# Performance work log

Hardware: AMD Instinct MI355X
Metric: run time of the kernel (lower is better)

## Reference

```python
import jax, jax.numpy as jnp
import numpy as np


def setup_inputs() -> dict:
    key = jax.random.key(0)
    ks = jax.random.split(key, 4)
    B, T, D, U = 64, 2048, 128, 128
    enc = jax.random.normal(ks[0], (B, T, D), dtype=jnp.float32)
    # Keras Dense default: glorot_uniform kernel, zero bias; use scaled normals here.
    W1_w = jax.random.normal(ks[1], (D, U), dtype=jnp.float32) / np.sqrt(D)
    W2_w = jax.random.normal(ks[2], (D, U), dtype=jnp.float32) / np.sqrt(D)
    V_w = jax.random.normal(ks[3], (U, 1), dtype=jnp.float32) / np.sqrt(U)
    return {
        "encoder_outputs": enc,
        "W1_w": W1_w,
        "W1_b": jnp.zeros((U,), jnp.float32),
        "W2_w": W2_w,
        "W2_b": jnp.zeros((U,), jnp.float32),
        "V_w": V_w,
        "V_b": jnp.zeros((1,), jnp.float32),
    }


def reference(encoder_outputs, W1_w, W1_b, W2_w, W2_b, V_w, V_b):
    # score = V(tanh(W1(x) + W2(x)))  -> [B, T, 1]
    # W1(x)+W2(x) == x @ (W1_w + W2_w) + (W1_b + W2_b); keep faithful but fused.
    h = jnp.tanh(jnp.einsum("btd,du->btu", encoder_outputs, W1_w) + W1_b
                 + jnp.einsum("btd,du->btu", encoder_outputs, W2_w) + W2_b)
    score = jnp.einsum("btu,uo->bto", h, V_w) + V_b  # [B, T, 1]
    attn = jax.nn.softmax(score, axis=1)             # softmax over sequence axis
    # context = sum_t attn[b,t,0] * x[b,t,:]
    context = jnp.einsum("bto,btd->bd", attn, encoder_outputs)
    return context
```

## Files before the change

kernel.cpp:

```cpp
#include <hip/hip_runtime.h>
#include <hip/hip_bf16.h>

#define DD 128
#define UU 128
#define SEQ_T 2048
#define ROWS 64
#define PART_STRIDE 132

typedef __attribute__((ext_vector_type(8))) short short8;
typedef __attribute__((ext_vector_type(4))) float f32x4;

__device__ __forceinline__ unsigned short f2bf(float f) {
  unsigned u = __float_as_uint(f);
  u += 0x7fffu + ((u >> 16) & 1u);
  return (unsigned short)(u >> 16);
}
__device__ __forceinline__ float bf2f(unsigned short s) {
  return __uint_as_float(((unsigned)s) << 16);
}
__device__ __forceinline__ float fast_tanh(float v) {
  float z = __expf(2.0f * v);
  return 1.0f - __fdividef(2.0f, z + 1.0f);
}

__global__ void prep_kernel(const float* __restrict__ W1w, const float* __restrict__ W1b,
                            const float* __restrict__ W2w, const float* __restrict__ W2b,
                            unsigned short* __restrict__ wt_g, float* __restrict__ bias_g)
{
  int i = blockIdx.x * 256 + threadIdx.x;
  int u = i >> 7, d = i & 127;
  float s = W1w[(size_t)d * UU + u] + W2w[(size_t)d * UU + u];
  wt_g[(size_t)u * DD + d] = f2bf(s);
  if (i < UU) bias_g[i] = W1b[i] + W2b[i];
}

__global__ __launch_bounds__(256, 4)
void fused_score_ctx(const float* __restrict__ x,
                     const unsigned short* __restrict__ wt_g,
                     const float* __restrict__ bias_g,
                     const float* __restrict__ Vw,
                     float* __restrict__ part)
{
  __shared__ __align__(16) unsigned short xs[ROWS * DD];
  __shared__ __align__(16) float spart[4][ROWS];
  __shared__ float slds[ROWS];
  __shared__ __align__(16) float pctx_red[4][DD];

  const int tid = threadIdx.x;
  const int blk = blockIdx.x;
  const int rowbase = blk * ROWS;
  const int w = tid >> 6, l = tid & 63, lx = l & 15, lq = l >> 4;

  float4 xr[8];
  #pragma unroll
  for (int it = 0; it < 4; ++it) {
    int F = tid + 256 * it;
    int row = F >> 4, g = F & 15;
    const float* src = x + (size_t)(rowbase + row) * DD + g * 8;
    xr[2 * it]     = *reinterpret_cast<const float4*>(src);
    xr[2 * it + 1] = *reinterpret_cast<const float4*>(src + 4);
  }

  short8 Bf[2][4];
  float vs[2], bs[2];
  #pragma unroll
  for (int nf = 0; nf < 2; ++nf) {
    const int u = 32 * w + 16 * nf + lx;
    vs[nf] = Vw[u];
    bs[nf] = bias_g[u];
    #pragma unroll
    for (int kf = 0; kf < 4; ++kf)
      Bf[nf][kf] = *reinterpret_cast<const short8*>(
          wt_g + (size_t)u * DD + 32 * kf + 8 * lq);
  }

  #pragma unroll
  for (int it = 0; it < 4; ++it) {
    int F = tid + 256 * it;
    int row = F >> 4, g = F & 15;
    float4 v0 = xr[2 * it], v1 = xr[2 * it + 1];
    short8 pk;
    pk[0] = (short)f2bf(v0.x); pk[1] = (short)f2bf(v0.y);
    pk[2] = (short)f2bf(v0.z); pk[3] = (short)f2bf(v0.w);
    pk[4] = (short)f2bf(v1.x); pk[5] = (short)f2bf(v1.y);
    pk[6] = (short)f2bf(v1.z); pk[7] = (short)f2bf(v1.w);
    *reinterpret_cast<short8*>(xs + row * DD + ((g ^ (row & 15)) << 3)) = pk;
  }
  __syncthreads();

  f32x4 acc[4][2];
  #pragma unroll
  for (int mf = 0; mf < 4; ++mf) {
    acc[mf][0] = (f32x4){0.f, 0.f, 0.f, 0.f};
    acc[mf][1] = (f32x4){0.f, 0.f, 0.f, 0.f};
  }
  #pragma unroll
  for (int kf = 0; kf < 4; ++kf) {
    const int gs8 = ((4 * kf + lq) ^ lx) << 3;
    #pragma unroll
    for (int mf = 0; mf < 4; ++mf) {
      short8 a = *reinterpret_cast<const short8*>(xs + (16 * mf + lx) * DD + gs8);
      acc[mf][0] = __builtin_amdgcn_mfma_f32_16x16x32_bf16(a, Bf[0][kf], acc[mf][0], 0, 0, 0);
      acc[mf][1] = __builtin_amdgcn_mfma_f32_16x16x32_bf16(a, Bf[1][kf], acc[mf][1], 0, 0, 0);
    }
  }

  #pragma unroll
  for (int mf = 0; mf < 4; ++mf) {
    #pragma unroll
    for (int r = 0; r < 4; ++r) {
      float p = vs[0] * fast_tanh(acc[mf][0][r] + bs[0])
              + vs[1] * fast_tanh(acc[mf][1][r] + bs[1]);
      p += __shfl_xor(p, 1);
      p += __shfl_xor(p, 2);
      p += __shfl_xor(p, 4);
      p += __shfl_xor(p, 8);
      if (lx == 0) spart[w][16 * mf + 4 * lq + r] = p;
    }
  }
  __syncthreads();

  float sv = (spart[0][l] + spart[1][l]) + (spart[2][l] + spart[3][l]);
  float m = sv;
  #pragma unroll
  for (int off = 1; off < 64; off <<= 1) m = fmaxf(m, __shfl_xor(m, off));
  float e = __expf(sv - m);
  float lsum = e;
  #pragma unroll
  for (int off = 1; off < 64; off <<= 1) lsum += __shfl_xor(lsum, off);
  if (w == 0) slds[l] = e;
  __syncthreads();

  {
    const int gd = tid & 15;
    const int tg = tid >> 4;
    float ca[8];
    #pragma unroll
    for (int e2 = 0; e2 < 8; ++e2) ca[e2] = 0.0f;
    #pragma unroll
    for (int k = 0; k < 4; ++k) {
      int t = tg * 4 + k;
      float wgt = slds[t];
      short8 xv = *reinterpret_cast<const short8*>(xs + t * DD + ((gd ^ (t & 15)) << 3));
      #pragma unroll
      for (int e2 = 0; e2 < 8; ++e2)
        ca[e2] = fmaf(wgt, bf2f((unsigned short)xv[e2]), ca[e2]);
    }
    #pragma unroll
    for (int e2 = 0; e2 < 8; ++e2) {
      ca[e2] += __shfl_xor(ca[e2], 16);
      ca[e2] += __shfl_xor(ca[e2], 32);
    }
    if ((l >> 4) == 0) {
      #pragma unroll
      for (int e2 = 0; e2 < 8; ++e2) pctx_red[w][gd * 8 + e2] = ca[e2];
    }
  }
  __syncthreads();

  float* prec = part + (size_t)blk * PART_STRIDE;
  if (tid < 128) {
    float c0 = (pctx_red[0][tid] + pctx_red[1][tid]) +
               (pctx_red[2][tid] + pctx_red[3][tid]);
    prec[4 + tid] = c0;
  }
  if (tid == 0) { prec[0] = m; prec[1] = lsum; }
}

__global__ void combine_kernel(const float* __restrict__ part,
                               float* __restrict__ out, int chunks)
{
  int b = blockIdx.x;
  int d = threadIdx.x;
  float mg = -3.0e38f;
  for (int i = 0; i < chunks; ++i)
    mg = fmaxf(mg, part[(size_t)(b * chunks + i) * PART_STRIDE]);
  float den = 0.0f, num = 0.0f;
  for (int i = 0; i < chunks; ++i) {
    const float* p = part + (size_t)(b * chunks + i) * PART_STRIDE;
    float sc = __expf(p[0] - mg);
    den = fmaf(sc, p[1], den);
    num = fmaf(sc, p[4 + d], num);
  }
  out[(size_t)b * DD + d] = __fdividef(num, den);
}

extern "C" void kernel_launch(void* const* d_in, const int* in_sizes, int n_in,
                              void* d_out, int out_size, void* d_ws, size_t ws_size,
                              hipStream_t stream)
{
  const float* x   = (const float*)d_in[0];
  const float* W1w = (const float*)d_in[1];
  const float* W1b = (const float*)d_in[2];
  const float* W2w = (const float*)d_in[3];
  const float* W2b = (const float*)d_in[4];
  const float* Vw  = (const float*)d_in[5];

  const int bt = in_sizes[0] / DD;
  const int nblk = bt / ROWS;
  const int B = bt / SEQ_T;
  const int chunks = SEQ_T / ROWS;

  const size_t part_bytes = (size_t)nblk * PART_STRIDE * sizeof(float);
  float* part = (float*)d_ws;
  unsigned short* wt_g = (unsigned short*)((char*)d_ws + part_bytes);
  float* bias_g = (float*)((char*)d_ws + part_bytes + 32768);

  prep_kernel<<<64, 256, 0, stream>>>(W1w, W1b, W2w, W2b, wt_g, bias_g);
  fused_score_ctx<<<nblk, 256, 0, stream>>>(x, wt_g, bias_g, Vw, part);
  combine_kernel<<<B, 128, 0, stream>>>(part, (float*)d_out, chunks);
}
```

Measured before the change: 44.16 us.

## Process two row tiles per block with prefetch of next tile into registers

Each block now handles two 64-row tiles, loading the second tile's global data into registers while the first tile's MFMA and softmax work proceeds, with a double-buffered LDS tile. This halves the block count and aims to hide global load latency and amortize weight-fragment loads. It also replaces the LDS softmax-weight buffer with a wave shuffle, switches to the builtin bf16 conversion, and lowers the occupancy hint to 3 blocks per CU. The per-tile barriers remain and LDS use doubles, which may reduce occupancy.

```diff
diff --git a/kernel.cpp b/kernel.cpp
--- a/kernel.cpp
+++ b/kernel.cpp
@@ -5,15 +5,14 @@
 #define UU 128
 #define SEQ_T 2048
 #define ROWS 64
+#define NTILE 2
 #define PART_STRIDE 132
 
 typedef __attribute__((ext_vector_type(8))) short short8;
 typedef __attribute__((ext_vector_type(4))) float f32x4;
 
 __device__ __forceinline__ unsigned short f2bf(float f) {
-  unsigned u = __float_as_uint(f);
-  u += 0x7fffu + ((u >> 16) & 1u);
-  return (unsigned short)(u >> 16);
+  return __builtin_bit_cast(unsigned short, __float2bfloat16(f));
 }
 __device__ __forceinline__ float bf2f(unsigned short s) {
   return __uint_as_float(((unsigned)s) << 16);
@@ -34,31 +33,33 @@
   if (i < UU) bias_g[i] = W1b[i] + W2b[i];
 }
 
-__global__ __launch_bounds__(256, 4)
+__global__ __launch_bounds__(256, 3)
 void fused_score_ctx(const float* __restrict__ x,
                      const unsigned short* __restrict__ wt_g,
                      const float* __restrict__ bias_g,
                      const float* __restrict__ Vw,
                      float* __restrict__ part)
 {
-  __shared__ __align__(16) unsigned short xs[ROWS * DD];
+  __shared__ __align__(16) unsigned short xs[2][ROWS * DD];
   __shared__ __align__(16) float spart[4][ROWS];
-  __shared__ float slds[ROWS];
   __shared__ __align__(16) float pctx_red[4][DD];
 
   const int tid = threadIdx.x;
   const int blk = blockIdx.x;
-  const int rowbase = blk * ROWS;
   const int w = tid >> 6, l = tid & 63, lx = l & 15, lq = l >> 4;
+  const int tau0 = blk * NTILE;
 
   float4 xr[8];
-  #pragma unroll
-  for (int it = 0; it < 4; ++it) {
-    int F = tid + 256 * it;
-    int row = F >> 4, g = F & 15;
-    const float* src = x + (size_t)(rowbase + row) * DD + g * 8;
-    xr[2 * it]     = *reinterpret_cast<const float4*>(src);
-    xr[2 * it + 1] = *reinterpret_cast<const float4*>(src + 4);
+  {
+    const float* xb = x + (size_t)tau0 * ROWS * DD;
+    #pragma unroll
+    for (int it = 0; it < 4; ++it) {
+      int F = tid + 256 * it;
+      int row = F >> 4, g = F & 15;
+      const float* src = xb + (size_t)row * DD + g * 8;
+      xr[2 * it]     = *reinterpret_cast<const float4*>(src);
+      xr[2 * it + 1] = *reinterpret_cast<const float4*>(src + 4);
+    }
   }
 
   short8 Bf[2][4];
@@ -74,97 +75,130 @@
           wt_g + (size_t)u * DD + 32 * kf + 8 * lq);
   }
 
+  short8 pk[4];
   #pragma unroll
   for (int it = 0; it < 4; ++it) {
-    int F = tid + 256 * it;
-    int row = F >> 4, g = F & 15;
     float4 v0 = xr[2 * it], v1 = xr[2 * it + 1];
-    short8 pk;
-    pk[0] = (short)f2bf(v0.x); pk[1] = (short)f2bf(v0.y);
-    pk[2] = (short)f2bf(v0.z); pk[3] = (short)f2bf(v0.w);
-    pk[4] = (short)f2bf(v1.x); pk[5] = (short)f2bf(v1.y);
-    pk[6] = (short)f2bf(v1.z); pk[7] = (short)f2bf(v1.w);
-    *reinterpret_cast<short8*>(xs + row * DD + ((g ^ (row & 15)) << 3)) = pk;
-  }
-  __syncthreads();
-
-  f32x4 acc[4][2];
-  #pragma unroll
-  for (int mf = 0; mf < 4; ++mf) {
-    acc[mf][0] = (f32x4){0.f, 0.f, 0.f, 0.f};
-    acc[mf][1] = (f32x4){0.f, 0.f, 0.f, 0.f};
-  }
-  #pragma unroll
-  for (int kf = 0; kf < 4; ++kf) {
-    const int gs8 = ((4 * kf + lq) ^ lx) << 3;
+    short8 p;
+    p[0] = (short)f2bf(v0.x); p[1] = (short)f2bf(v0.y);
+    p[2] = (short)f2bf(v0.z); p[3] = (short)f2bf(v0.w);
+    p[4] = (short)f2bf(v1.x); p[5] = (short)f2bf(v1.y);
+    p[6] = (short)f2bf(v1.z); p[7] = (short)f2bf(v1.w);
+    pk[it] = p;
+  }
+
+  for (int t = 0; t < NTILE; ++t) {
+    unsigned short* xb = xs[t & 1];
+
+    #pragma unroll
+    for (int it = 0; it < 4; ++it) {
+      int F = tid + 256 * it;
+      int row = F >> 4, g = F & 15;
+      *reinterpret_cast<short8*>(xb + row * DD + ((g ^ (row & 15)) << 3)) = pk[it];
+    }
+    __syncthreads();
+
+    if (t + 1 < NTILE) {
+      const float* nb = x + (size_t)(tau0 + t + 1) * ROWS * DD;
+      #pragma unroll
+      for (int it = 0; it < 4; ++it) {
+        int F = tid + 256 * it;
+        int row = F >> 4, g = F & 15;
+        const float* src = nb + (size_t)row * DD + g * 8;
+        xr[2 * it]     = *reinterpret_cast<const float4*>(src);
+        xr[2 * it + 1] = *reinterpret_cast<const float4*>(src + 4);
+      }
+    }
+
+    f32x4 acc[4][2];
     #pragma unroll
     for (int mf = 0; mf < 4; ++mf) {
-      short8 a = *reinterpret_cast<const short8*>(xs + (16 * mf + lx) * DD + gs8);
-      acc[mf][0] = __builtin_amdgcn_mfma_f32_16x16x32_bf16(a, Bf[0][kf], acc[mf][0], 0, 0, 0);
-      acc[mf][1] = __builtin_amdgcn_mfma_f32_16x16x32_bf16(a, Bf[1][kf], acc[mf][1], 0, 0, 0);
-    }
-  }
-
-  #pragma unroll
-  for (int mf = 0; mf < 4; ++mf) {
-    #pragma unroll
-    for (int r = 0; r < 4; ++r) {
-      float p = vs[0] * fast_tanh(acc[mf][0][r] + bs[0])
-              + vs[1] * fast_tanh(acc[mf][1][r] + bs[1]);
-      p += __shfl_xor(p, 1);
-      p += __shfl_xor(p, 2);
-      p += __shfl_xor(p, 4);
-      p += __shfl_xor(p, 8);
-      if (lx == 0) spart[w][16 * mf + 4 * lq + r] = p;
-    }
-  }
-  __syncthreads();
-
-  float sv = (spart[0][l] + spart[1][l]) + (spart[2][l] + spart[3][l]);
-  float m = sv;
-  #pragma unroll
-  for (int off = 1; off < 64; off <<= 1) m = fmaxf(m, __shfl_xor(m, off));
-  float e = __expf(sv - m);
-  float lsum = e;
-  #pragma unroll
-  for (int off = 1; off < 64; off <<= 1) lsum += __shfl_xor(lsum, off);
-  if (w == 0) slds[l] = e;
-  __syncthreads();
-
-  {
-    const int gd = tid & 15;
-    const int tg = tid >> 4;
-    float ca[8];
-    #pragma unroll
-    for (int e2 = 0; e2 < 8; ++e2) ca[e2] = 0.0f;
-    #pragma unroll
-    for (int k = 0; k < 4; ++k) {
-      int t = tg * 4 + k;
-      float wgt = slds[t];
-      short8 xv = *reinterpret_cast<const short8*>(xs + t * DD + ((gd ^ (t & 15)) << 3));
-      #pragma unroll
-      for (int e2 = 0; e2 < 8; ++e2)
-        ca[e2] = fmaf(wgt, bf2f((unsigned short)xv[e2]), ca[e2]);
-    }
-    #pragma unroll
-    for (int e2 = 0; e2 < 8; ++e2) {
-      ca[e2] += __shfl_xor(ca[e2], 16);
-      ca[e2] += __shfl_xor(ca[e2], 32);
-    }
-    if ((l >> 4) == 0) {
-      #pragma unroll
-      for (int e2 = 0; e2 < 8; ++e2) pctx_red[w][gd * 8 + e2] = ca[e2];
-    }
-  }
-  __syncthreads();
-
-  float* prec = part + (size_t)blk * PART_STRIDE;
-  if (tid < 128) {
-    float c0 = (pctx_red[0][tid] + pctx_red[1][tid]) +
-               (pctx_red[2][tid] + pctx_red[3][tid]);
-    prec[4 + tid] = c0;
-  }
-  if (tid == 0) { prec[0] = m; prec[1] = lsum; }
+      acc[mf][0] = (f32x4){0.f, 0.f, 0.f, 0.f};
+      acc[mf][1] = (f32x4){0.f, 0.f, 0.f, 0.f};
+    }
+    #pragma unroll
+    for (int kf = 0; kf < 4; ++kf) {
+      const int gs8 = ((4 * kf + lq) ^ lx) << 3;
+      #pragma unroll
+      for (int mf = 0; mf < 4; ++mf) {
+        short8 a = *reinterpret_cast<const short8*>(xb + (16 * mf + lx) * DD + gs8);
+        acc[mf][0] = __builtin_amdgcn_mfma_f32_16x16x32_bf16(a, Bf[0][kf], acc[mf][0], 0, 0, 0);
+        acc[mf][1] = __builtin_amdgcn_mfma_f32_16x16x32_bf16(a, Bf[1][kf], acc[mf][1], 0, 0, 0);
+      }
+    }
+
+    #pragma unroll
+    for (int mf = 0; mf < 4; ++mf) {
+      #pragma unroll
+      for (int r = 0; r < 4; ++r) {
+        float p = vs[0] * fast_tanh(acc[mf][0][r] + bs[0])
+                + vs[1] * fast_tanh(acc[mf][1][r] + bs[1]);
+        p += __shfl_xor(p, 1);
+        p += __shfl_xor(p, 2);
+        p += __shfl_xor(p, 4);
+        p += __shfl_xor(p, 8);
+        if (lx == 0) spart[w][16 * mf + 4 * lq + r] = p;
+      }
+    }
+
+    if (t + 1 < NTILE) {
+      #pragma unroll
+      for (int it = 0; it < 4; ++it) {
+        float4 v0 = xr[2 * it], v1 = xr[2 * it + 1];
+        short8 p;
+        p[0] = (short)f2bf(v0.x); p[1] = (short)f2bf(v0.y);
+        p[2] = (short)f2bf(v0.z); p[3] = (short)f2bf(v0.w);
+        p[4] = (short)f2bf(v1.x); p[5] = (short)f2bf(v1.y);
+        p[6] = (short)f2bf(v1.z); p[7] = (short)f2bf(v1.w);
+        pk[it] = p;
+      }
+    }
+    __syncthreads();
+
+    float sv = (spart[0][l] + spart[1][l]) + (spart[2][l] + spart[3][l]);
+    float m = sv;
+    #pragma unroll
+    for (int off = 1; off < 64; off <<= 1) m = fmaxf(m, __shfl_xor(m, off));
+    float e = __expf(sv - m);
+    float lsum = e;
+    #pragma unroll
+    for (int off = 1; off < 64; off <<= 1) lsum += __shfl_xor(lsum, off);
+
+    {
+      const int gd = l & 15;
+      float ca[8];
+      #pragma unroll
+      for (int e2 = 0; e2 < 8; ++e2) ca[e2] = 0.0f;
+      #pragma unroll
+      for (int k = 0; k < 4; ++k) {
+        int row = 16 * w + 4 * (l >> 4) + k;
+        float wgt = __shfl(e, row);
+        short8 xv = *reinterpret_cast<const short8*>(
+            xb + row * DD + ((gd ^ (row & 15)) << 3));
+        #pragma unroll
+        for (int e2 = 0; e2 < 8; ++e2)
+          ca[e2] = fmaf(wgt, bf2f((unsigned short)xv[e2]), ca[e2]);
+      }
+      #pragma unroll
+      for (int e2 = 0; e2 < 8; ++e2) {
+        ca[e2] += __shfl_xor(ca[e2], 16);
+        ca[e2] += __shfl_xor(ca[e2], 32);
+      }
+      if ((l >> 4) == 0) {
+        #pragma unroll
+        for (int e2 = 0; e2 < 8; ++e2) pctx_red[w][gd * 8 + e2] = ca[e2];
+      }
+    }
+    __syncthreads();
+
+    float* prec = part + (size_t)(tau0 + t) * PART_STRIDE;
+    if (tid < 128) {
+      float c0 = (pctx_red[0][tid] + pctx_red[1][tid]) +
+                 (pctx_red[2][tid] + pctx_red[3][tid]);
+      prec[4 + tid] = c0;
+    }
+    if (tid == 0) { prec[0] = m; prec[1] = lsum; }
+  }
 }
 
 __global__ void combine_kernel(const float* __restrict__ part,
@@ -197,11 +231,12 @@
   const float* Vw  = (const float*)d_in[5];
 
   const int bt = in_sizes[0] / DD;
-  const int nblk = bt / ROWS;
+  const int ntiles = bt / ROWS;
+  const int nblk = ntiles / NTILE;
   const int B = bt / SEQ_T;
   const int chunks = SEQ_T / ROWS;
 
-  const size_t part_bytes = (size_t)nblk * PART_STRIDE * sizeof(float);
+  const size_t part_bytes = (size_t)ntiles * PART_STRIDE * sizeof(float);
   float* part = (float*)d_ws;
   unsigned short* wt_g = (unsigned short*)((char*)d_ws + part_bytes);
   float* bias_g = (float*)((char*)d_ws + part_bytes + 32768);
```

Result: slower. 59.69 us (+35.2%).

## Split fused score/context kernel into scores, alpha, and context passes with atomics

Applied to the files above, without the earlier changes.

Replaces the single fused kernel plus per-batch combine with three kernels. The first computes scores and per-chunk softmax stats and writes them to workspace. A small kernel turns the chunk stats into rescale factors and zeroes the output. A context kernel then re-reads x in fp32, applies the weights, and accumulates into the output with atomics. This drops the serial 32-chunk combine loop and uses full fp32 x for the context, at the cost of reading x from HBM twice, an extra launch, and atomic accumulation.

```diff
diff --git a/kernel.cpp b/kernel.cpp
--- a/kernel.cpp
+++ b/kernel.cpp
@@ -5,7 +5,7 @@
 #define UU 128
 #define SEQ_T 2048
 #define ROWS 64
-#define PART_STRIDE 132
+#define NCHUNK 32
 
 typedef __attribute__((ext_vector_type(8))) short short8;
 typedef __attribute__((ext_vector_type(4))) float f32x4;
@@ -22,6 +22,13 @@
   float z = __expf(2.0f * v);
   return 1.0f - __fdividef(2.0f, z + 1.0f);
 }
+
+#define WT_OFF   0
+#define BIAS_OFF 33280
+#define MW_OFF   33792
+#define LW_OFF   41984
+#define EW_OFF   50176
+#define AW_OFF   574464
 
 __global__ void prep_kernel(const float* __restrict__ W1w, const float* __restrict__ W1b,
                             const float* __restrict__ W2w, const float* __restrict__ W2b,
@@ -35,16 +42,15 @@
 }
 
 __global__ __launch_bounds__(256, 4)
-void fused_score_ctx(const float* __restrict__ x,
-                     const unsigned short* __restrict__ wt_g,
-                     const float* __restrict__ bias_g,
-                     const float* __restrict__ Vw,
-                     float* __restrict__ part)
+void scores_kernel(const float* __restrict__ x,
+                   const unsigned short* __restrict__ wt_g,
+                   const float* __restrict__ bias_g,
+                   const float* __restrict__ Vw,
+                   float* __restrict__ mw, float* __restrict__ lw,
+                   float* __restrict__ e_ws)
 {
   __shared__ __align__(16) unsigned short xs[ROWS * DD];
   __shared__ __align__(16) float spart[4][ROWS];
-  __shared__ float slds[ROWS];
-  __shared__ __align__(16) float pctx_red[4][DD];
 
   const int tid = threadIdx.x;
   const int blk = blockIdx.x;
@@ -128,61 +134,80 @@
   float lsum = e;
   #pragma unroll
   for (int off = 1; off < 64; off <<= 1) lsum += __shfl_xor(lsum, off);
-  if (w == 0) slds[l] = e;
+
+  if (w == 0) e_ws[(size_t)blk * ROWS + l] = e;
+  if (tid == 0) { mw[blk] = m; lw[blk] = lsum; }
+}
+
+__global__ void alpha_kernel(const float* __restrict__ mw, const float* __restrict__ lw,
+                             float* __restrict__ aw, float* __restrict__ out)
+{
+  const int b = blockIdx.x;
+  const int t = threadIdx.x;
+  if (t < 128) out[(size_t)b * DD + t] = 0.0f;
+
+  if (t < 64) {
+    float mi = (t < NCHUNK) ? mw[b * NCHUNK + t] : -3.0e38f;
+    float li = (t < NCHUNK) ? lw[b * NCHUNK + t] : 0.0f;
+    float M = mi;
+    #pragma unroll
+    for (int off = 1; off < 32; off <<= 1) M = fmaxf(M, __shfl_xor(M, off));
+    float term = (t < NCHUNK) ? __expf(mi - M) * li : 0.0f;
+    float L = term;
+    #pragma unroll
+    for (int off = 1; off < 32; off <<= 1) L += __shfl_xor(L, off);
+    if (t < NCHUNK) aw[b * NCHUNK + t] = __fdividef(__expf(mi - M), L);
+  }
+}
+
+__global__ __launch_bounds__(256, 8)
+void context_kernel(const float* __restrict__ x,
+                    const float* __restrict__ e_ws, const float* __restrict__ aw,
+                    float* __restrict__ out)
+{
+  __shared__ __align__(16) float pctx[4][DD];
+
+  const int tid = threadIdx.x;
+  const int blk = blockIdx.x;
+  const int rowbase = blk * ROWS;
+  const int b = blk >> 5;
+  const int c = blk & 31;
+  const int w = tid >> 6, l = tid & 63;
+  const int gd = tid & 15;
+  const int tg = tid >> 4;
+
+  const float alpha = aw[b * NCHUNK + c];
+
+  float ca[8];
+  #pragma unroll
+  for (int e2 = 0; e2 < 8; ++e2) ca[e2] = 0.0f;
+  #pragma unroll
+  for (int k = 0; k < 4; ++k) {
+    const int row = tg * 4 + k;
+    const float wgt = alpha * e_ws[(size_t)blk * ROWS + row];
+    const float* src = x + (size_t)(rowbase + row) * DD + gd * 8;
+    const float4 v0 = *reinterpret_cast<const float4*>(src);
+    const float4 v1 = *reinterpret_cast<const float4*>(src + 4);
+    ca[0] = fmaf(wgt, v0.x, ca[0]); ca[1] = fmaf(wgt, v0.y, ca[1]);
+    ca[2] = fmaf(wgt, v0.z, ca[2]); ca[3] = fmaf(wgt, v0.w, ca[3]);
+    ca[4] = fmaf(wgt, v1.x, ca[4]); ca[5] = fmaf(wgt, v1.y, ca[5]);
+    ca[6] = fmaf(wgt, v1.z, ca[6]); ca[7] = fmaf(wgt, v1.w, ca[7]);
+  }
+  #pragma unroll
+  for (int e2 = 0; e2 < 8; ++e2) {
+    ca[e2] += __shfl_xor(ca[e2], 16);
+    ca[e2] += __shfl_xor(ca[e2], 32);
+  }
+  if (l < 16) {
+    #pragma unroll
+    for (int e2 = 0; e2 < 8; ++e2) pctx[w][l * 8 + e2] = ca[e2];
+  }
   __syncthreads();
 
-  {
-    const int gd = tid & 15;
-    const int tg = tid >> 4;
-    float ca[8];
-    #pragma unroll
-    for (int e2 = 0; e2 < 8; ++e2) ca[e2] = 0.0f;
-    #pragma unroll
-    for (int k = 0; k < 4; ++k) {
-      int t = tg * 4 + k;
-      float wgt = slds[t];
-      short8 xv = *reinterpret_cast<const short8*>(xs + t * DD + ((gd ^ (t & 15)) << 3));
-      #pragma unroll
-      for (int e2 = 0; e2 < 8; ++e2)
-        ca[e2] = fmaf(wgt, bf2f((unsigned short)xv[e2]), ca[e2]);
-    }
-    #pragma unroll
-    for (int e2 = 0; e2 < 8; ++e2) {
-      ca[e2] += __shfl_xor(ca[e2], 16);
-      ca[e2] += __shfl_xor(ca[e2], 32);
-    }
-    if ((l >> 4) == 0) {
-      #pragma unroll
-      for (int e2 = 0; e2 < 8; ++e2) pctx_red[w][gd * 8 + e2] = ca[e2];
-    }
-  }
-  __syncthreads();
-
-  float* prec = part + (size_t)blk * PART_STRIDE;
   if (tid < 128) {
-    float c0 = (pctx_red[0][tid] + pctx_red[1][tid]) +
-               (pctx_red[2][tid] + pctx_red[3][tid]);
-    prec[4 + tid] = c0;
-  }
-  if (tid == 0) { prec[0] = m; prec[1] = lsum; }
-}
-
-__global__ void combine_kernel(const float* __restrict__ part,
-                               float* __restrict__ out, int chunks)
-{
-  int b = blockIdx.x;
-  int d = threadIdx.x;
-  float mg = -3.0e38f;
-  for (int i = 0; i < chunks; ++i)
-    mg = fmaxf(mg, part[(size_t)(b * chunks + i) * PART_STRIDE]);
-  float den = 0.0f, num = 0.0f;
-  for (int i = 0; i < chunks; ++i) {
-    const float* p = part + (size_t)(b * chunks + i) * PART_STRIDE;
-    float sc = __expf(p[0] - mg);
-    den = fmaf(sc, p[1], den);
-    num = fmaf(sc, p[4 + d], num);
-  }
-  out[(size_t)b * DD + d] = __fdividef(num, den);
+    float c0 = (pctx[0][tid] + pctx[1][tid]) + (pctx[2][tid] + pctx[3][tid]);
+    atomicAdd(&out[(size_t)b * DD + tid], c0);
+  }
 }
 
 extern "C" void kernel_launch(void* const* d_in, const int* in_sizes, int n_in,
@@ -199,14 +224,18 @@
   const int bt = in_sizes[0] / DD;
   const int nblk = bt / ROWS;
   const int B = bt / SEQ_T;
-  const int chunks = SEQ_T / ROWS;
-
-  const size_t part_bytes = (size_t)nblk * PART_STRIDE * sizeof(float);
-  float* part = (float*)d_ws;
-  unsigned short* wt_g = (unsigned short*)((char*)d_ws + part_bytes);
-  float* bias_g = (float*)((char*)d_ws + part_bytes + 32768);
+
+  char* ws = (char*)d_ws;
+  unsigned short* wt_g = (unsigned short*)(ws + WT_OFF);
+  float* bias_g = (float*)(ws + BIAS_OFF);
+  float* mw   = (float*)(ws + MW_OFF);
+  float* lw   = (float*)(ws + LW_OFF);
+  float* e_ws = (float*)(ws + EW_OFF);
+  float* aw   = (float*)(ws + AW_OFF);
+  float* out  = (float*)d_out;
 
   prep_kernel<<<64, 256, 0, stream>>>(W1w, W1b, W2w, W2b, wt_g, bias_g);
-  fused_score_ctx<<<nblk, 256, 0, stream>>>(x, wt_g, bias_g, Vw, part);
-  combine_kernel<<<B, 128, 0, stream>>>(part, (float*)d_out, chunks);
-}
+  scores_kernel<<<nblk, 256, 0, stream>>>(x, wt_g, bias_g, Vw, mw, lw, e_ws);
+  alpha_kernel<<<B, 128, 0, stream>>>(mw, lw, aw, out);
+  context_kernel<<<nblk, 256, 0, stream>>>(x, e_ws, aw, out);
+}
```

New measurement: 40.75 us. 1.08x faster.
